# Kernel tuning notes

Measured on AMD Instinct MI355X. Metric: run time of the kernel, lower is better.

## Reference

```python
import jax, jax.numpy as jnp
import numpy as np

N_WORD = 50000
N_DOC = 10000
E_WW = 800000
E_WD = 320000


def _sage(h_src, h_dst, src, dst, n_dst, W_self, W_neigh, b):
    # DGL SAGEConv('mean'): fc_self(h_dst) + fc_neigh(mean_{u in N(v)} h_u) + bias
    ones = jnp.ones((src.shape[0],), dtype=h_src.dtype)
    deg = jax.ops.segment_sum(ones, dst, num_segments=n_dst)            # [n_dst]
    agg = jax.ops.segment_sum(h_src[src], dst, num_segments=n_dst)      # [n_dst, d]
    mean = agg / jnp.maximum(deg, 1.0)[:, None]                          # zero for isolated
    return h_dst @ W_self + mean @ W_neigh + b


def _layer(xw, xd, edges, Ws, Wn, b):
    (ww_s, ww_d, wwr_s, wwr_d, wd_s, wd_d, wdr_s, wdr_d) = edges
    # relations targeting 'word': word2word, word2wordr, word2documentr
    h_ww = _sage(xw, xw, ww_s, ww_d, N_WORD, Ws[0], Wn[0], b[0])
    h_wwr = _sage(xw, xw, wwr_s, wwr_d, N_WORD, Ws[1], Wn[1], b[1])
    h_wdr = _sage(xd, xw, wdr_s, wdr_d, N_WORD, Ws[3], Wn[3], b[3])
    # relation targeting 'document': word2document
    h_wd = _sage(xw, xd, wd_s, wd_d, N_DOC, Ws[2], Wn[2], b[2])
    # HeteroGraphConv aggregate='stack' then torch.sum(dim=1) == sum over relations; then relu
    return jax.nn.relu(h_ww + h_wwr + h_wdr), jax.nn.relu(h_wd)


def setup_inputs() -> dict:
    key = jax.random.key(0)
    ks = jax.random.split(key, 20)
    d_in, d_h = 256, 128
    inp = {
        "x_word": jax.random.normal(ks[0], (N_WORD, d_in), jnp.float32),
        "x_doc": jax.random.normal(ks[1], (N_DOC, d_in), jnp.float32),
        "ww_src": jax.random.randint(ks[2], (E_WW,), 0, N_WORD, jnp.int32),
        "ww_dst": jax.random.randint(ks[3], (E_WW,), 0, N_WORD, jnp.int32),
        "wwr_src": jax.random.randint(ks[4], (E_WW,), 0, N_WORD, jnp.int32),
        "wwr_dst": jax.random.randint(ks[5], (E_WW,), 0, N_WORD, jnp.int32),
        "wd_src": jax.random.randint(ks[6], (E_WD,), 0, N_WORD, jnp.int32),
        "wd_dst": jax.random.randint(ks[7], (E_WD,), 0, N_DOC, jnp.int32),
        "wdr_src": jax.random.randint(ks[8], (E_WD,), 0, N_DOC, jnp.int32),
        "wdr_dst": jax.random.randint(ks[9], (E_WD,), 0, N_WORD, jnp.int32),
        "Wself1": jax.random.normal(ks[10], (4, d_in, d_h), jnp.float32) * (1.0 / np.sqrt(d_in)),
        "Wneigh1": jax.random.normal(ks[11], (4, d_in, d_h), jnp.float32) * (1.0 / np.sqrt(d_in)),
        "b1": jnp.zeros((4, d_h), jnp.float32),
        "Wself2": jax.random.normal(ks[12], (4, d_h, d_h), jnp.float32) * (1.0 / np.sqrt(d_h)),
        "Wneigh2": jax.random.normal(ks[13], (4, d_h, d_h), jnp.float32) * (1.0 / np.sqrt(d_h)),
        "b2": jnp.zeros((4, d_h), jnp.float32),
        "lin_w": jax.random.normal(ks[14], (1, d_h), jnp.float32) * (1.0 / np.sqrt(d_h)),
        "lin_b": jnp.ones((1,), jnp.float32),
    }
    return inp


def reference(x_word, x_doc, ww_src, ww_dst, wwr_src, wwr_dst, wd_src, wd_dst,
              wdr_src, wdr_dst, Wself1, Wneigh1, b1, Wself2, Wneigh2, b2, lin_w, lin_b):
    edges = (ww_src, ww_dst, wwr_src, wwr_dst, wd_src, wd_dst, wdr_src, wdr_dst)
    xw, xd = _layer(x_word, x_doc, edges, Wself1, Wneigh1, b1)
    xw, xd = _layer(xw, xd, edges, Wself2, Wneigh2, b2)
    out_w = jax.nn.sigmoid(xw @ lin_w.T + lin_b)  # [N_WORD, 1]
    out_d = jax.nn.sigmoid(xd @ lin_w.T + lin_b)  # [N_DOC, 1]
    return out_w, out_d
```

## Files before the change

### kernel.cpp

```cpp
#include <hip/hip_runtime.h>
#include <math.h>

#define N_WORD 50000
#define N_DOC  10000
#define E_WW   800000
#define E_WD   320000
#define D_IN   256
#define D_H    128

#define NPB    256
#define NBK_W  196
#define NBK_D  40
#define BKT    (3 * NBK_W + NBK_D)
#define EPB    4096
#define NBLK_WW 196
#define NBLK_WD 79
#define NBLK_TOT (2 * NBLK_WW + 2 * NBLK_WD)
#define PACK_BLKS 145

#define CAP_WW  4736
#define CAP_WDR 2176
#define CAP_WD  8960

#define WSTRIP ((N_WORD + 63) / 64)
#define DSTRIP ((N_DOC + 63) / 64)
#define NSTRIP (WSTRIP + DSTRIP)

typedef __attribute__((ext_vector_type(8))) short short8;
typedef __attribute__((ext_vector_type(4))) float f32x4;

__device__ inline unsigned short f2bf(float f) {
  unsigned u = __float_as_uint(f);
  u = (u + 0x7fffu + ((u >> 16) & 1u)) >> 16;
  return (unsigned short)u;
}

struct G6 { const short* B[6]; unsigned short* C[6]; };

template <int ABF, int K>
__device__ void gemm_body(const void* __restrict__ Aw, const void* __restrict__ Ad,
                          const G6& g, int blk) {
  constexpr int KT = K >> 5;
  int wid = threadIdx.x >> 6, lane = threadIdx.x & 63;
  const void* A; int M, row0, h0, h1;
  if (blk < WSTRIP) { A = Aw; M = N_WORD; row0 = blk << 6; h0 = 0; h1 = 4; }
  else { A = Ad; M = N_DOC; row0 = (blk - WSTRIP) << 6; h0 = 4; h1 = 6; }
  int r = lane & 15, quad = lane >> 4;
  int m0 = row0 + wid * 16;
  int mA = m0 + r; if (mA >= M) mA = M - 1;
  short8 afr[KT];
  if (ABF) {
    const short* ap = (const short*)A + (size_t)mA * K + quad * 8;
#pragma unroll
    for (int kt = 0; kt < KT; ++kt) afr[kt] = *(const short8*)(ap + kt * 32);
  } else {
    const float* ap = (const float*)A + (size_t)mA * K + quad * 8;
#pragma unroll
    for (int kt = 0; kt < KT; ++kt) {
      float4 a0 = *(const float4*)(ap + kt * 32);
      float4 a1 = *(const float4*)(ap + kt * 32 + 4);
      short8 v;
      v[0] = (short)f2bf(a0.x); v[1] = (short)f2bf(a0.y);
      v[2] = (short)f2bf(a0.z); v[3] = (short)f2bf(a0.w);
      v[4] = (short)f2bf(a1.x); v[5] = (short)f2bf(a1.y);
      v[6] = (short)f2bf(a1.z); v[7] = (short)f2bf(a1.w);
      afr[kt] = v;
    }
  }
  for (int h = h0; h < h1; ++h) {
    const short* Bp = g.B[h];
    f32x4 acc[8];
#pragma unroll
    for (int nt = 0; nt < 8; ++nt) acc[nt] = (f32x4){0.f, 0.f, 0.f, 0.f};
#pragma unroll
    for (int kt = 0; kt < KT; ++kt) {
      const short* bbase = Bp + ((size_t)kt * 4096) + lane * 8;
#pragma unroll
      for (int nt = 0; nt < 8; ++nt) {
        short8 bf = *(const short8*)(bbase + (size_t)nt * 512);
        acc[nt] = __builtin_amdgcn_mfma_f32_16x16x32_bf16(afr[kt], bf, acc[nt], 0, 0, 0);
      }
    }
    unsigned short* C = g.C[h];
#pragma unroll
    for (int nt = 0; nt < 8; ++nt)
#pragma unroll
      for (int rr = 0; rr < 4; ++rr) {
        int row = m0 + quad * 4 + rr;
        if (row < M) C[(size_t)row * 128 + nt * 16 + r] = f2bf(acc[nt][rr]);
      }
  }
}

__global__ __launch_bounds__(256) void prep_kernel(
    const float* __restrict__ Ws1, const float* __restrict__ Wn1,
    const float* __restrict__ Ws2, const float* __restrict__ Wn2,
    short* __restrict__ Bp1, short* __restrict__ Bp2,
    const float* __restrict__ b1, const float* __restrict__ b2,
    float* __restrict__ bs1, float* __restrict__ bs2, int* __restrict__ bcnt) {
  int b = blockIdx.x;
  if (b == PACK_BLKS) {
    for (int i = threadIdx.x; i < BKT; i += 256) bcnt[i] = 0;
    return;
  }
  int tid = b * 256 + threadIdx.x;
  const int L1T = 6 * 4096;
  const int L2T = 6 * 2048;
  if (tid >= L1T + L2T) {
    int t = tid - (L1T + L2T);
    if (t < 128) bs1[t] = b1[t] + b1[128 + t] + b1[384 + t];
    else if (t < 256) { int u = t - 128; bs2[u] = b2[u] + b2[128 + u] + b2[384 + u]; }
    return;
  }
  const float *src0, *src1 = nullptr, *src2 = nullptr;
  short* dstp;
  int kt, nt, lane;
  if (tid < L1T) {
    int mat = tid / 4096, rem = tid % 4096;
    kt = rem / 512; nt = (rem / 64) % 8; lane = rem % 64;
    const int W1 = 256 * 128;
    if (mat == 0) { src0 = Ws1; src1 = Ws1 + W1; src2 = Ws1 + 3 * W1; }
    else if (mat <= 4) src0 = Wn1 + (size_t)(mat - 1) * W1;
    else src0 = Ws1 + 2 * W1;
    dstp = Bp1 + (size_t)mat * W1 + ((size_t)(kt * 8 + nt) * 64 + lane) * 8;
  } else {
    int t2 = tid - L1T;
    int mat = t2 / 2048, rem = t2 % 2048;
    kt = rem / 512; nt = (rem / 64) % 8; lane = rem % 64;
    const int W2 = 128 * 128;
    if (mat == 0) { src0 = Ws2; src1 = Ws2 + W2; src2 = Ws2 + 3 * W2; }
    else if (mat <= 4) src0 = Wn2 + (size_t)(mat - 1) * W2;
    else src0 = Ws2 + 2 * W2;
    dstp = Bp2 + (size_t)mat * W2 + ((size_t)(kt * 8 + nt) * 64 + lane) * 8;
  }
  int n = nt * 16 + (lane & 15);
  int kb = kt * 32 + (lane >> 4) * 8;
  short8 v;
#pragma unroll
  for (int j = 0; j < 8; ++j) {
    float f = src0[(size_t)(kb + j) * 128 + n];
    if (src1) f += src1[(size_t)(kb + j) * 128 + n] + src2[(size_t)(kb + j) * 128 + n];
    v[j] = (short)f2bf(f);
  }
  *(short8*)dstp = v;
}

__device__ inline void rel_map(int b, const int* wwd, const int* wwrd, const int* wdrd,
                               const int* wdd, const int*& dst, int& E, int& gbase, int& lb) {
  if (b < NBLK_WW) { dst = wwd; E = E_WW; gbase = 0; lb = b; }
  else if (b < 2 * NBLK_WW) { dst = wwrd; E = E_WW; gbase = NBK_W; lb = b - NBLK_WW; }
  else if (b < 2 * NBLK_WW + NBLK_WD) { dst = wdrd; E = E_WD; gbase = 2 * NBK_W; lb = b - 2 * NBLK_WW; }
  else { dst = wdd; E = E_WD; gbase = 3 * NBK_W; lb = b - 2 * NBLK_WW - NBLK_WD; }
}

__global__ __launch_bounds__(256, 4) void bin_gemm1(
    const int* wws, const int* wwd, const int* wwrs, const int* wwrd,
    const int* wdrs, const int* wdrd, const int* wds, const int* wdd,
    int* bcnt, unsigned* st_ww, unsigned* st_wwr, unsigned* st_wdr, unsigned* st_wd,
    const float* __restrict__ Aw, const float* __restrict__ Ad, G6 g) {
  __shared__ int h[4][NBK_W], wb[4][NBK_W], cur[4][NBK_W];
  int b = blockIdx.x;
  if (b >= NBLK_TOT) {
    gemm_body<0, 256>(Aw, Ad, g, b - NBLK_TOT);
    return;
  }
  const int* dst; int E, gbase, lb;
  rel_map(b, wwd, wwrd, wdrd, wdd, dst, E, gbase, lb);
  const int* src; unsigned* st; int cap;
  if (b < NBLK_WW) { src = wws; st = st_ww; cap = CAP_WW; }
  else if (b < 2 * NBLK_WW) { src = wwrs; st = st_wwr; cap = CAP_WW; }
  else if (b < 2 * NBLK_WW + NBLK_WD) { src = wdrs; st = st_wdr; cap = CAP_WDR; }
  else { src = wds; st = st_wd; cap = CAP_WD; }
  int tid = threadIdx.x;
  int wave = tid >> 6;
  for (int i = tid; i < 4 * NBK_W; i += 256) { ((int*)h)[i] = 0; ((int*)cur)[i] = 0; }
  __syncthreads();
  int e0 = lb * EPB;
  int dcache[EPB / 256];
#pragma unroll
  for (int k = 0; k < EPB / 256; ++k) {
    int i = e0 + k * 256 + tid;
    int d = (i < E) ? dst[i] : -1;
    dcache[k] = d;
    if (d >= 0) atomicAdd(&h[wave][d >> 8], 1);
  }
  __syncthreads();
  if (tid < NBK_W) {
    int t0 = h[0][tid], t1 = h[1][tid], t2 = h[2][tid], t3 = h[3][tid];
    int tot = t0 + t1 + t2 + t3;
    int base = tot ? atomicAdd(&bcnt[gbase + tid], tot) : 0;
    wb[0][tid] = base;
    wb[1][tid] = base + t0;
    wb[2][tid] = base + t0 + t1;
    wb[3][tid] = base + t0 + t1 + t2;
  }
  __syncthreads();
#pragma unroll
  for (int k = 0; k < EPB / 256; ++k) {
    int d = dcache[k];
    if (d >= 0) {
      int i = e0 + k * 256 + tid;
      int bk = d >> 8;
      int l = atomicAdd(&cur[wave][bk], 1);
      st[(size_t)bk * cap + wb[wave][bk] + l] =
          (unsigned)(src[i] & 0xFFFF) | ((unsigned)(d & (NPB - 1)) << 16);
    }
  }
}

struct CSRB {
  const unsigned *st_ww, *st_wwr, *st_wdr, *st_wd;
  unsigned short *c_ww, *c_wwr, *c_wdr, *c_wd;
  int *rp_ww, *rp_wwr, *rp_wdr, *rp_wd;
  const int* bcnt;
};

__global__ __launch_bounds__(256) void place_kernel(CSRB q) {
  __shared__ int cnt[256], off[256], sm[256];
  int g = blockIdx.x;
  const unsigned* st; unsigned short* csr; int* rp; int relFirst, relLast, n, cap, Etot;
  if (g < NBK_W)            { st = q.st_ww;  csr = q.c_ww;  rp = q.rp_ww;  relFirst = 0;         relLast = NBK_W - 1;     n = N_WORD; cap = CAP_WW;  Etot = E_WW; }
  else if (g < 2 * NBK_W)   { st = q.st_wwr; csr = q.c_wwr; rp = q.rp_wwr; relFirst = NBK_W;     relLast = 2 * NBK_W - 1; n = N_WORD; cap = CAP_WW;  Etot = E_WW; }
  else if (g < 3 * NBK_W)   { st = q.st_wdr; csr = q.c_wdr; rp = q.rp_wdr; relFirst = 2 * NBK_W; relLast = 3 * NBK_W - 1; n = N_WORD; cap = CAP_WDR; Etot = E_WD; }
  else                      { st = q.st_wd;  csr = q.c_wd;  rp = q.rp_wd;  relFirst = 3 * NBK_W; relLast = BKT - 1;       n = N_DOC;  cap = CAP_WD;  Etot = E_WD; }
  int cb = g - relFirst;
  int tid = threadIdx.x;
  int v = (tid < cb) ? q.bcnt[relFirst + tid] : 0;
  sm[tid] = v;
  __syncthreads();
  for (int o = 128; o > 0; o >>= 1) {
    if (tid < o) sm[tid] += sm[tid + o];
    __syncthreads();
  }
  int bstart = sm[0];
  if (g == relLast && tid == 0) rp[n] = Etot;
  __syncthreads();
  int node_base = cb << 8;
  int node_cnt = n - node_base; if (node_cnt > NPB) node_cnt = NPB;
  int ecnt = q.bcnt[g];
  const unsigned* w = st + (size_t)cb * cap;
  cnt[tid] = 0;
  __syncthreads();
  for (int j = tid; j < ecnt; j += 256) atomicAdd(&cnt[w[j] >> 16], 1);
  __syncthreads();
  int c = cnt[tid];
  sm[tid] = c;
  __syncthreads();
  for (int o = 1; o < 256; o <<= 1) {
    int add = (tid >= o) ? sm[tid - o] : 0;
    __syncthreads();
    sm[tid] += add;
    __syncthreads();
  }
  int ex = sm[tid] - c;
  off[tid] = ex;
  if (tid < node_cnt) rp[node_base + tid] = bstart + ex;
  __syncthreads();
  for (int j = tid; j < ecnt; j += 256) {
    unsigned e = w[j];
    int p = atomicAdd(&off[e >> 16], 1);
    csr[bstart + p] = (unsigned short)(e & 0xFFFFu);
  }
}

__global__ __launch_bounds__(256, 6) void gemm2_kernel(
    const void* __restrict__ Aw, const void* __restrict__ Ad, G6 g) {
  gemm_body<1, 128>(Aw, Ad, g, blockIdx.x);
}

__device__ inline void accum_rel(const unsigned* __restrict__ y,
                                 const unsigned short* __restrict__ csr,
                                 int beg, int end, int lane, float& f0, float& f1) {
  float a0 = 0.f, a1 = 0.f;
  for (int base = beg; base < end; base += 64) {
    int cnt = end - base; if (cnt > 64) cnt = 64;
    int ld = base + lane; if (ld >= end) ld = end - 1;
    int idx = csr[ld];
    int j = 0;
    for (; j + 7 < cnt; j += 8) {
      unsigned u[8];
#pragma unroll
      for (int k = 0; k < 8; ++k) {
        int s = __builtin_amdgcn_readlane(idx, j + k);
        u[k] = y[((size_t)s << 6) + lane];
      }
#pragma unroll
      for (int k = 0; k < 8; ++k) {
        a0 += __uint_as_float(u[k] << 16);
        a1 += __uint_as_float(u[k] & 0xffff0000u);
      }
    }
    for (; j < cnt; ++j) {
      int s = __builtin_amdgcn_readlane(idx, j);
      unsigned uu = y[((size_t)s << 6) + lane];
      a0 += __uint_as_float(uu << 16);
      a1 += __uint_as_float(uu & 0xffff0000u);
    }
  }
  int deg = end - beg;
  float inv = 1.0f / (float)(deg > 1 ? deg : 1);
  f0 += a0 * inv;
  f1 += a1 * inv;
}

__global__ __launch_bounds__(256) void gather_all(
    const unsigned* __restrict__ y_ww, const unsigned* __restrict__ y_wwr,
    const unsigned* __restrict__ y_wdr, const unsigned* __restrict__ y_wd,
    const unsigned short* __restrict__ c_ww, const unsigned short* __restrict__ c_wwr,
    const unsigned short* __restrict__ c_wdr, const unsigned short* __restrict__ c_wd,
    const int* __restrict__ r_ww, const int* __restrict__ r_wwr,
    const int* __restrict__ r_wdr, const int* __restrict__ r_wd,
    const unsigned* __restrict__ tW, const unsigned* __restrict__ tD,
    const float* __restrict__ bW, const float* __restrict__ bD,
    const float* __restrict__ lw, const float* __restrict__ lb,
    unsigned* __restrict__ oW16, unsigned* __restrict__ oD16,
    float* __restrict__ oF, int mode) {
  int gn = (blockIdx.x << 2) + (threadIdx.x >> 6);
  if (gn >= N_WORD + N_DOC) return;
  int lane = threadIdx.x & 63;
  float f0, f1;
  if (gn < N_WORD) {
    int node = gn;
    unsigned tu = tW[((size_t)node << 6) + lane];
    f0 = __uint_as_float(tu << 16);
    f1 = __uint_as_float(tu & 0xffff0000u);
    accum_rel(y_ww, c_ww, r_ww[node], r_ww[node + 1], lane, f0, f1);
    accum_rel(y_wwr, c_wwr, r_wwr[node], r_wwr[node + 1], lane, f0, f1);
    accum_rel(y_wdr, c_wdr, r_wdr[node], r_wdr[node + 1], lane, f0, f1);
    float2 bv = ((const float2*)bW)[lane];
    f0 = fmaxf(f0 + bv.x, 0.f);
    f1 = fmaxf(f1 + bv.y, 0.f);
    if (mode == 1) {
      oW16[((size_t)node << 6) + lane] = (unsigned)f2bf(f0) | ((unsigned)f2bf(f1) << 16);
    } else {
      float2 lv = ((const float2*)lw)[lane];
      float s = f0 * lv.x + f1 * lv.y;
#pragma unroll
      for (int off = 32; off > 0; off >>= 1) s += __shfl_xor(s, off);
      if (lane == 0) oF[node] = 1.0f / (1.0f + expf(-(s + lb[0])));
    }
  } else {
    int node = gn - N_WORD;
    unsigned tu = tD[((size_t)node << 6) + lane];
    f0 = __uint_as_float(tu << 16);
    f1 = __uint_as_float(tu & 0xffff0000u);
    accum_rel(y_wd, c_wd, r_wd[node], r_wd[node + 1], lane, f0, f1);
    float2 bv = ((const float2*)bD)[lane];
    f0 = fmaxf(f0 + bv.x, 0.f);
    f1 = fmaxf(f1 + bv.y, 0.f);
    if (mode == 1) {
      oD16[((size_t)node << 6) + lane] = (unsigned)f2bf(f0) | ((unsigned)f2bf(f1) << 16);
    } else {
      float2 lv = ((const float2*)lw)[lane];
      float s = f0 * lv.x + f1 * lv.y;
#pragma unroll
      for (int off = 32; off > 0; off >>= 1) s += __shfl_xor(s, off);
      if (lane == 0) oF[N_WORD + node] = 1.0f / (1.0f + expf(-(s + lb[0])));
    }
  }
}

extern "C" void kernel_launch(void* const* d_in, const int* in_sizes, int n_in,
                              void* d_out, int out_size, void* d_ws, size_t ws_size,
                              hipStream_t stream) {
  const float* xw      = (const float*)d_in[0];
  const float* xd      = (const float*)d_in[1];
  const int*   ww_src  = (const int*)d_in[2];
  const int*   ww_dst  = (const int*)d_in[3];
  const int*   wwr_src = (const int*)d_in[4];
  const int*   wwr_dst = (const int*)d_in[5];
  const int*   wd_src  = (const int*)d_in[6];
  const int*   wd_dst  = (const int*)d_in[7];
  const int*   wdr_src = (const int*)d_in[8];
  const int*   wdr_dst = (const int*)d_in[9];
  const float* Ws1     = (const float*)d_in[10];
  const float* Wn1     = (const float*)d_in[11];
  const float* b1      = (const float*)d_in[12];
  const float* Ws2     = (const float*)d_in[13];
  const float* Wn2     = (const float*)d_in[14];
  const float* b2      = (const float*)d_in[15];
  const float* lin_w   = (const float*)d_in[16];
  const float* lin_b   = (const float*)d_in[17];
  float* out = (float*)d_out;

  char* p = (char*)d_ws;
  auto alloc = [&](size_t nbytes) {
    char* r = p;
    p += (nbytes + 255) & ~(size_t)255;
    return r;
  };
  unsigned* twA  = (unsigned*)alloc((size_t)N_WORD * D_H * 2);
  unsigned* tdA  = (unsigned*)alloc((size_t)N_DOC * D_H * 2);
  unsigned* xw1B = (unsigned*)alloc((size_t)N_WORD * D_H * 2);
  unsigned* xd1B = (unsigned*)alloc((size_t)N_DOC * D_H * 2);
  unsigned* yB0 = (unsigned*)alloc((size_t)N_WORD * D_H * 2);
  unsigned* yB1 = (unsigned*)alloc((size_t)N_WORD * D_H * 2);
  unsigned* yB2 = (unsigned*)alloc((size_t)N_WORD * D_H * 2);
  unsigned* ydB = (unsigned*)alloc((size_t)N_DOC * D_H * 2);
  unsigned short* csr_ww  = (unsigned short*)alloc((size_t)E_WW * 2);
  unsigned short* csr_wwr = (unsigned short*)alloc((size_t)E_WW * 2);
  unsigned short* csr_wdr = (unsigned short*)alloc((size_t)E_WD * 2);
  unsigned short* csr_wd  = (unsigned short*)alloc((size_t)E_WD * 2);
  int* rp_ww  = (int*)alloc((size_t)(N_WORD + 1) * 4);
  int* rp_wwr = (int*)alloc((size_t)(N_WORD + 1) * 4);
  int* rp_wdr = (int*)alloc((size_t)(N_WORD + 1) * 4);
  int* rp_wd  = (int*)alloc((size_t)(N_DOC + 1) * 4);
  short* Bp1 = (short*)alloc((size_t)6 * 256 * 128 * 2);
  short* Bp2 = (short*)alloc((size_t)6 * 128 * 128 * 2);
  int* bcnt  = (int*)alloc((size_t)BKT * 4);
  float* bs1 = (float*)alloc(D_H * 4);
  float* bs2 = (float*)alloc(D_H * 4);
  unsigned* yBX = (unsigned*)alloc((size_t)N_WORD * D_H * 2);
  unsigned* st_ww  = yB0;
  unsigned* st_wwr = st_ww + (size_t)NBK_W * CAP_WW;
  unsigned* st_wdr = yB1;
  unsigned* st_wd  = st_wdr + (size_t)NBK_W * CAP_WDR;

  const int W1 = 256 * 128;
  const int W2 = 128 * 128;

  prep_kernel<<<PACK_BLKS + 1, 256, 0, stream>>>(
      Ws1, Wn1, Ws2, Wn2, Bp1, Bp2, b1, b2, bs1, bs2, bcnt);

  G6 g1;
  g1.B[0] = Bp1 + 0 * W1; g1.C[0] = (unsigned short*)twA;
  g1.B[1] = Bp1 + 1 * W1; g1.C[1] = (unsigned short*)yB2;
  g1.B[2] = Bp1 + 2 * W1; g1.C[2] = (unsigned short*)xw1B;
  g1.B[3] = Bp1 + 3 * W1; g1.C[3] = (unsigned short*)yBX;
  g1.B[4] = Bp1 + 5 * W1; g1.C[4] = (unsigned short*)tdA;
  g1.B[5] = Bp1 + 4 * W1; g1.C[5] = (unsigned short*)ydB;
  bin_gemm1<<<NBLK_TOT + NSTRIP, 256, 0, stream>>>(
      ww_src, ww_dst, wwr_src, wwr_dst, wdr_src, wdr_dst, wd_src, wd_dst,
      bcnt, st_ww, st_wwr, st_wdr, st_wd, xw, xd, g1);

  CSRB q;
  q.st_ww = st_ww; q.st_wwr = st_wwr; q.st_wdr = st_wdr; q.st_wd = st_wd;
  q.c_ww = csr_ww; q.c_wwr = csr_wwr; q.c_wdr = csr_wdr; q.c_wd = csr_wd;
  q.rp_ww = rp_ww; q.rp_wwr = rp_wwr; q.rp_wdr = rp_wdr; q.rp_wd = rp_wd;
  q.bcnt = bcnt;
  place_kernel<<<BKT, 256, 0, stream>>>(q);

  gather_all<<<(N_WORD + N_DOC + 3) / 4, 256, 0, stream>>>(
      yB2, xw1B, ydB, yBX, csr_ww, csr_wwr, csr_wdr, csr_wd,
      rp_ww, rp_wwr, rp_wdr, rp_wd, twA, tdA, bs1, b1 + 256,
      lin_w, lin_b, yB0, xd1B, nullptr, 1);

  G6 g2;
  g2.B[0] = Bp2 + 0 * W2; g2.C[0] = (unsigned short*)twA;
  g2.B[1] = Bp2 + 1 * W2; g2.C[1] = (unsigned short*)yB2;
  g2.B[2] = Bp2 + 2 * W2; g2.C[2] = (unsigned short*)xw1B;
  g2.B[3] = Bp2 + 3 * W2; g2.C[3] = (unsigned short*)yBX;
  g2.B[4] = Bp2 + 5 * W2; g2.C[4] = (unsigned short*)tdA;
  g2.B[5] = Bp2 + 4 * W2; g2.C[5] = (unsigned short*)ydB;
  gemm2_kernel<<<NSTRIP, 256, 0, stream>>>(yB0, xd1B, g2);

  gather_all<<<(N_WORD + N_DOC + 3) / 4, 256, 0, stream>>>(
      yB2, xw1B, ydB, yBX, csr_ww, csr_wwr, csr_wdr, csr_wd,
      rp_ww, rp_wwr, rp_wdr, rp_wd, twA, tdA, bs2, b2 + 256,
      lin_w, lin_b, nullptr, nullptr, out, 2);
}
```

Before: 408.8 us.

## Stage binned edges in LDS for coalesced bucket writes, doubling edges per block

Each binning block now handles twice as many edges and first sorts its edges by bucket into an LDS buffer, using a block-wide prefix scan over the bucket histogram. It then writes the buffer out contiguously, so global stores within each bucket are grouped instead of scattered one by one. This costs an extra LDS pass, a larger LDS footprint (about 36KB), and more registers for dcache, which may lower occupancy for the fused gemm blocks that share this kernel.

```diff
diff --git a/kernel.cpp b/kernel.cpp
--- a/kernel.cpp
+++ b/kernel.cpp
@@ -12,9 +12,9 @@
 #define NBK_W  196
 #define NBK_D  40
 #define BKT    (3 * NBK_W + NBK_D)
-#define EPB    4096
-#define NBLK_WW 196
-#define NBLK_WD 79
+#define EPB    8192
+#define NBLK_WW 98
+#define NBLK_WD 40
 #define NBLK_TOT (2 * NBLK_WW + 2 * NBLK_WD)
 #define PACK_BLKS 145
 
@@ -153,12 +153,21 @@
   else { dst = wdd; E = E_WD; gbase = 3 * NBK_W; lb = b - 2 * NBLK_WW - NBLK_WD; }
 }
 
+struct BinLDS {
+  unsigned buf[EPB];
+  int hist[NBK_W];
+  int lofs[NBK_W];
+  int gofs[NBK_W];
+  int lcur[NBK_W];
+  int sm[256];
+};
+
 __global__ __launch_bounds__(256, 4) void bin_gemm1(
     const int* wws, const int* wwd, const int* wwrs, const int* wwrd,
     const int* wdrs, const int* wdrd, const int* wds, const int* wdd,
     int* bcnt, unsigned* st_ww, unsigned* st_wwr, unsigned* st_wdr, unsigned* st_wd,
     const float* __restrict__ Aw, const float* __restrict__ Ad, G6 g) {
-  __shared__ int h[4][NBK_W], wb[4][NBK_W], cur[4][NBK_W];
+  __shared__ BinLDS L;
   int b = blockIdx.x;
   if (b >= NBLK_TOT) {
     gemm_body<0, 256>(Aw, Ad, g, b - NBLK_TOT);
@@ -172,27 +181,36 @@
   else if (b < 2 * NBLK_WW + NBLK_WD) { src = wdrs; st = st_wdr; cap = CAP_WDR; }
   else { src = wds; st = st_wd; cap = CAP_WD; }
   int tid = threadIdx.x;
-  int wave = tid >> 6;
-  for (int i = tid; i < 4 * NBK_W; i += 256) { ((int*)h)[i] = 0; ((int*)cur)[i] = 0; }
-  __syncthreads();
   int e0 = lb * EPB;
+  int ecnt = E - e0; if (ecnt > EPB) ecnt = EPB;
+  if (tid < NBK_W) L.hist[tid] = 0;
+  __syncthreads();
   int dcache[EPB / 256];
 #pragma unroll
   for (int k = 0; k < EPB / 256; ++k) {
     int i = e0 + k * 256 + tid;
     int d = (i < E) ? dst[i] : -1;
     dcache[k] = d;
-    if (d >= 0) atomicAdd(&h[wave][d >> 8], 1);
-  }
-  __syncthreads();
-  if (tid < NBK_W) {
-    int t0 = h[0][tid], t1 = h[1][tid], t2 = h[2][tid], t3 = h[3][tid];
-    int tot = t0 + t1 + t2 + t3;
-    int base = tot ? atomicAdd(&bcnt[gbase + tid], tot) : 0;
-    wb[0][tid] = base;
-    wb[1][tid] = base + t0;
-    wb[2][tid] = base + t0 + t1;
-    wb[3][tid] = base + t0 + t1 + t2;
+    if (d >= 0) atomicAdd(&L.hist[d >> 8], 1);
+  }
+  __syncthreads();
+  {
+    int v = (tid < NBK_W) ? L.hist[tid] : 0;
+    L.sm[tid] = v;
+    __syncthreads();
+    for (int o = 1; o < 256; o <<= 1) {
+      int add = (tid >= o) ? L.sm[tid - o] : 0;
+      __syncthreads();
+      L.sm[tid] += add;
+      __syncthreads();
+    }
+    if (tid < NBK_W) {
+      int ex = L.sm[tid] - v;
+      L.lofs[tid] = ex;
+      L.lcur[tid] = ex;
+      int base = v ? atomicAdd(&bcnt[gbase + tid], v) : 0;
+      L.gofs[tid] = (int)((size_t)tid * cap) + base - ex;
+    }
   }
   __syncthreads();
 #pragma unroll
@@ -201,9 +219,18 @@
     if (d >= 0) {
       int i = e0 + k * 256 + tid;
       int bk = d >> 8;
-      int l = atomicAdd(&cur[wave][bk], 1);
-      st[(size_t)bk * cap + wb[wave][bk] + l] =
-          (unsigned)(src[i] & 0xFFFF) | ((unsigned)(d & (NPB - 1)) << 16);
+      int p = atomicAdd(&L.lcur[bk], 1);
+      L.buf[p] = ((unsigned)bk << 24) | ((unsigned)(d & 255) << 16) |
+                 (unsigned)(src[i] & 0xFFFF);
+    }
+  }
+  __syncthreads();
+#pragma unroll
+  for (int k = 0; k < EPB / 256; ++k) {
+    int p = k * 256 + tid;
+    if (p < ecnt) {
+      unsigned e = L.buf[p];
+      st[L.gofs[e >> 24] + p] = e & 0x00FFFFFFu;
     }
   }
 }
```

Result: faster. 400.0 us (-2.2%).
